# Optimization experiments

Measured on AMD Instinct MI355X. Metric: run time of the kernel, lower is better.

## Reference

```python
import jax, jax.numpy as jnp
import numpy as np
import math

B, C, H, W = 16, 128, 64, 64

def _conv3(x, w, b):
    # 3x3 conv, padding=1 (SAME), NCHW / OIHW
    y = jax.lax.conv_general_dilated(x, w, window_strides=(1, 1), padding='SAME',
                                     dimension_numbers=('NCHW', 'OIHW', 'NCHW'))
    return y + b[None, :, None, None]

def setup_inputs() -> dict:
    key = jax.random.key(0)
    ks = jax.random.split(key, 12)
    s = 0.02
    inp = {
        'F_in': jax.random.normal(ks[0], (B, C, H, W), dtype=jnp.float32),
        'Pspe': jax.random.normal(ks[1], (B, C, C), dtype=jnp.float32),
        'q_w': jax.random.normal(ks[2], (C, C, 3, 3), dtype=jnp.float32) * s,
        'q_b': jnp.zeros((C,), dtype=jnp.float32),
        'k_w': jax.random.normal(ks[3], (C, C, 3, 3), dtype=jnp.float32) * s,
        'k_b': jnp.zeros((C,), dtype=jnp.float32),
        'v_w': jax.random.normal(ks[4], (C, C, 3, 3), dtype=jnp.float32) * s,
        'v_b': jnp.zeros((C,), dtype=jnp.float32),
        'f1_w': jax.random.normal(ks[5], (C, C, 3, 3), dtype=jnp.float32) * s,
        'f1_b': jnp.zeros((C,), dtype=jnp.float32),
        'f2_w': jax.random.normal(ks[6], (C, C, 3, 3), dtype=jnp.float32) * s,
        'f2_b': jnp.zeros((C,), dtype=jnp.float32),
    }
    return inp

def reference(F_in, Pspe, q_w, q_b, k_w, k_b, v_w, v_b, f1_w, f1_b, f2_w, f2_b):
    b, c, h, w = F_in.shape
    hw = h * w
    Qm = _conv3(F_in, q_w, q_b)
    Km = _conv3(F_in, k_w, k_b)
    Vm = _conv3(F_in, v_w, v_b)
    # (B,C,H,W) -> (B,HW,C)
    Q = jnp.transpose(Qm, (0, 2, 3, 1)).reshape(b, hw, c)
    K = jnp.transpose(Km, (0, 2, 3, 1)).reshape(b, hw, c)
    V = jnp.transpose(Vm, (0, 2, 3, 1)).reshape(b, hw, c)
    # channel-wise attention: (B,C,C) = K^T Q, contracting over HW
    attn_logits = jnp.einsum('bnc,bnd->bcd', K, Q) / math.sqrt(hw)
    A = jax.nn.softmax(attn_logits, axis=-1)
    M = jnp.einsum('bce,bed->bcd', Pspe, A)         # prompt fusion
    F3 = jnp.einsum('bnc,bcd->bnd', V, M)           # (B,HW,C)
    F3_map = jnp.transpose(F3.reshape(b, h, w, c), (0, 3, 1, 2))
    # MScanBlock is not defined in the provided source -> identity
    F_ssm = F3_map
    ffn = _conv3(jax.nn.gelu(_conv3(F_ssm, f1_w, f1_b), approximate=False), f2_w, f2_b)
    return F_ssm + ffn
```

## Files before the change

### kernel.cpp

```cpp
#include <hip/hip_runtime.h>
#include <cmath>

typedef unsigned short u16;
typedef __bf16 bf16x8 __attribute__((ext_vector_type(8)));
typedef float f32x4 __attribute__((ext_vector_type(4)));

__device__ __forceinline__ u16 f2bf(float f) {
  unsigned u = __float_as_uint(f);
  u += 0x7fffu + ((u >> 16) & 1u);
  return (u16)(u >> 16);
}
__device__ __forceinline__ float bf2f(u16 h) {
  return __uint_as_float(((unsigned)h) << 16);
}
__device__ __forceinline__ f32x4 mfma_bf16(bf16x8 a, bf16x8 b, f32x4 c) {
  return __builtin_amdgcn_mfma_f32_16x16x32_bf16(a, b, c, 0, 0, 0);
}
__device__ __forceinline__ float gelu_exact(float x) {
  return 0.5f * x * (1.0f + erff(x * 0.70710678118654752440f));
}

#define ROWB 272

__global__ __launch_bounds__(256) void pack_xw(
    const float* __restrict__ Fin, u16* __restrict__ X,
    const float* __restrict__ w0, const float* __restrict__ w1,
    const float* __restrict__ w2, const float* __restrict__ w3,
    const float* __restrict__ w4, u16* __restrict__ Wpk) {
  __shared__ float T[64 * 129];
  const int tid = threadIdx.x;
  if (blockIdx.x < 1024) {
    const int b = blockIdx.x >> 6, y = blockIdx.x & 63;
#pragma unroll
    for (int i = 0; i < 32; ++i) {
      int idx = tid + i * 256;
      int c = idx >> 6, x = idx & 63;
      T[x * 129 + c] = Fin[(size_t)(b * 128 + c) * 4096 + y * 64 + x];
    }
    __syncthreads();
#pragma unroll
    for (int i = 0; i < 4; ++i) {
      int chunk = tid + i * 256;
      int x = chunk >> 4;
      int c0 = (chunk & 15) * 8;
      u16 tmp[8];
#pragma unroll
      for (int e = 0; e < 8; ++e) tmp[e] = f2bf(T[x * 129 + c0 + e]);
      *reinterpret_cast<uint4*>(X + ((size_t)((b * 64 + y) * 64 + x) * 128 + c0)) =
          *reinterpret_cast<const uint4*>(tmp);
    }
  } else {
    int gid = (blockIdx.x - 1024) * 256 + tid;
    int lane = gid & 63;
    int nblk = (gid >> 6) & 7;
    int step = (gid >> 9) % 36;
    int conv = gid / (512 * 36);
    if (conv >= 5) return;
    const float* w = conv == 0 ? w0 : conv == 1 ? w1 : conv == 2 ? w2 : conv == 3 ? w3 : w4;
    int tap = step >> 2, cc = step & 3;
    int dy = tap / 3, dx = tap % 3;
    int co = nblk * 16 + (lane & 15);
    int ci0 = cc * 32 + (lane >> 4) * 8;
    u16 tmp[8];
#pragma unroll
    for (int e = 0; e < 8; ++e)
      tmp[e] = f2bf(w[((size_t)(co * 128 + ci0 + e) * 3 + dy) * 3 + dx]);
    size_t off = ((size_t)conv * 36 * 8 * 64 + (size_t)((step * 8 + nblk) * 64 + lane)) * 8;
    *reinterpret_cast<uint4*>(Wpk + off) = *reinterpret_cast<const uint4*>(tmp);
  }
}

__device__ __forceinline__ void stage_tile(const u16* __restrict__ Xin, char* Xsb,
                                           int tid, int b, int y0) {
#pragma unroll
  for (int i = 0; i < 16; ++i) {
    int j = tid + i * 256;
    int row = j >> 4;
    int c16 = j & 15;
    int ys = row >> 6, x = row & 63;
    int ysrc = y0 - 1 + ys;
    uint4 val = make_uint4(0u, 0u, 0u, 0u);
    if ((unsigned)ysrc < 64u)
      val = *reinterpret_cast<const uint4*>(
          Xin + ((size_t)((b * 64 + ysrc) * 64 + x) * 128 + c16 * 8));
    *reinterpret_cast<uint4*>(Xsb + (ys * 66 + x + 1) * ROWB + c16 * 16) = val;
  }
  if (tid < 128) {
    int ys = tid >> 5, side = (tid >> 4) & 1, c16 = tid & 15;
    int xs = side ? 65 : 0;
    *reinterpret_cast<uint4*>(Xsb + (ys * 66 + xs) * ROWB + c16 * 16) =
        make_uint4(0u, 0u, 0u, 0u);
  }
}

__global__ __launch_bounds__(256, 2) void conv_qkv(
    const u16* __restrict__ Xin, const u16* __restrict__ Wp,
    const float* __restrict__ qb, const float* __restrict__ kb,
    const float* __restrict__ vb, u16* __restrict__ QP,
    u16* __restrict__ KP, u16* __restrict__ Vout) {
  __shared__ alignas(16) char Xsb[4 * 66 * ROWB];
  const int tid = threadIdx.x;
  const int lane = tid & 63;
  const int wv = tid >> 6;
  const int wm = wv >> 1, wn = wv & 1;
  int mt = blockIdx.x;
  mt = (mt & 7) * 128 + (mt >> 3);
  const int b = mt >> 6;
  const int r = mt & 63;
  const int yp = r >> 1;
  const int nh = r & 1;
  const int y0 = yp * 2;

  stage_tile(Xin, Xsb, tid, b, y0);
  __syncthreads();

  f32x4 acc[3][4][2];
#pragma unroll
  for (int c = 0; c < 3; ++c)
#pragma unroll
    for (int i = 0; i < 4; ++i)
#pragma unroll
      for (int j = 0; j < 2; ++j) acc[c][i][j] = f32x4{0.f, 0.f, 0.f, 0.f};

  const int lm = lane & 15, lq = lane >> 4;
  const int abase = lm * ROWB + lq * 16;
  const u16* wb = Wp + (size_t)(((nh * 4 + wn * 2) * 64) + lane) * 8;

  auto loada = [&](bf16x8 (&d)[4], int s) {
    int tap = s >> 2, cc = s & 3;
    int dy = (tap * 11) >> 5;
    int dx = tap - dy * 3;
    int roff = ((wm + dy) * 66 + dx) * ROWB + cc * 64 + abase;
#pragma unroll
    for (int i = 0; i < 4; ++i)
      d[i] = *reinterpret_cast<const bf16x8*>(Xsb + roff + i * (16 * ROWB));
  };
  auto loadb = [&](bf16x8 (&d)[6], int s) {
#pragma unroll
    for (int cv = 0; cv < 3; ++cv)
#pragma unroll
      for (int j = 0; j < 2; ++j)
        d[cv * 2 + j] = *reinterpret_cast<const bf16x8*>(
            wb + (size_t)cv * 147456 + (size_t)s * 4096 + j * 512);
  };
  auto step = [&](bf16x8 (&a)[4], bf16x8 (&bm)[6]) {
#pragma unroll
    for (int cv = 0; cv < 3; ++cv)
#pragma unroll
      for (int i = 0; i < 4; ++i)
#pragma unroll
        for (int j = 0; j < 2; ++j)
          acc[cv][i][j] = mfma_bf16(a[i], bm[cv * 2 + j], acc[cv][i][j]);
  };

  bf16x8 a0[4], a1[4], a2[4], b0[6], b1[6], b2[6];
  loada(a0, 0); loadb(b0, 0);
  loada(a1, 1); loadb(b1, 1);
  loada(a2, 2); loadb(b2, 2);
#pragma unroll 1
  for (int s = 0; s < 36; s += 3) {
    step(a0, b0);
    if (s + 3 < 36) { loada(a0, s + 3); loadb(b0, s + 3); }
    step(a1, b1);
    if (s + 4 < 36) { loada(a1, s + 4); loadb(b1, s + 4); }
    step(a2, b2);
    if (s + 5 < 36) { loada(a2, s + 5); loadb(b2, s + 5); }
  }

  __syncthreads();

  u16* T = reinterpret_cast<u16*>(Xsb);
#pragma unroll
  for (int cv = 0; cv < 2; ++cv) {
    const float* bias = cv == 0 ? qb : kb;
    u16* OutB = cv == 0 ? QP : KP;
#pragma unroll
    for (int i = 0; i < 4; ++i)
#pragma unroll
      for (int j = 0; j < 2; ++j) {
        int nloc = wn * 32 + j * 16 + lm;
        float bs = bias[nh * 64 + nloc];
#pragma unroll
        for (int rr = 0; rr < 4; ++rr) {
          int m = wm * 64 + i * 16 + lq * 4 + rr;
          T[nloc * 136 + m] = f2bf(acc[cv][i][j][rr] + bs);
        }
      }
    __syncthreads();
#pragma unroll
    for (int it = 0; it < 4; ++it) {
      int item = tid + it * 256;
      int l = item & 63, cbl = (item >> 6) & 3, ksl = item >> 8;
      int c = cbl * 16 + (l & 15);
      int mloc = ksl * 32 + (l >> 4) * 8;
      int ks = yp * 4 + ksl, cb = nh * 4 + cbl;
      *reinterpret_cast<uint4*>(
          OutB + (size_t)(((b * 128 + ks) * 8 + cb) * 64 + l) * 8) =
          *reinterpret_cast<const uint4*>(T + c * 136 + mloc);
    }
    __syncthreads();
  }

  u16* Tv = reinterpret_cast<u16*>(Xsb);
#pragma unroll
  for (int i = 0; i < 4; ++i)
#pragma unroll
    for (int j = 0; j < 2; ++j) {
      int nloc = wn * 32 + j * 16 + lm;
      float bs = vb[nh * 64 + nloc];
#pragma unroll
      for (int rr = 0; rr < 4; ++rr) {
        int m = wm * 64 + i * 16 + lq * 4 + rr;
        Tv[m * 72 + nloc] = f2bf(acc[2][i][j][rr] + bs);
      }
    }
  __syncthreads();
  {
    int rr = tid >> 1, q = tid & 1;
    const uint4* src = reinterpret_cast<const uint4*>(Tv + rr * 72 + q * 32);
    uint4* dst = reinterpret_cast<uint4*>(
        Vout + ((size_t)((b * 32 + yp) * 128 + rr) * 128 + nh * 64 + q * 32));
#pragma unroll
    for (int k = 0; k < 4; ++k) dst[k] = src[k];
  }
}

template <int MODE>
__global__ __launch_bounds__(256, 2) void conv_gemm(
    const u16* __restrict__ Xin, const u16* __restrict__ Wp,
    const float* __restrict__ bias, u16* __restrict__ OutB,
    float* __restrict__ OutF, const u16* __restrict__ Vin,
    const u16* __restrict__ Mpk) {
  __shared__ alignas(16) char Xsb[4 * 66 * ROWB];
  const int tid = threadIdx.x;
  const int lane = tid & 63;
  const int wv = tid >> 6;
  const int wm = wv >> 1, wn = wv & 1;
  int mt = blockIdx.x;
  mt = (mt & 7) * 64 + (mt >> 3);
  const int b = mt >> 5;
  const int y0 = (mt & 31) * 2;

  stage_tile(Xin, Xsb, tid, b, y0);
  __syncthreads();

  f32x4 acc[4][4];
#pragma unroll
  for (int i = 0; i < 4; ++i)
#pragma unroll
    for (int j = 0; j < 4; ++j) acc[i][j] = f32x4{0.f, 0.f, 0.f, 0.f};

  const int lm = lane & 15, lq = lane >> 4;
  const int abase = lm * ROWB + lq * 16;
  const u16* wb = Wp + (MODE == 1 ? (size_t)b * 147456 : (size_t)0) +
                  (size_t)((wn * 4 * 64) + lane) * 8;

  auto loada = [&](bf16x8 (&d)[4], int s) {
    int tap = s >> 2, cc = s & 3;
    int dy = (tap * 11) >> 5;
    int dx = tap - dy * 3;
    int roff = ((wm + dy) * 66 + dx) * ROWB + cc * 64 + abase;
#pragma unroll
    for (int i = 0; i < 4; ++i)
      d[i] = *reinterpret_cast<const bf16x8*>(Xsb + roff + i * (16 * ROWB));
  };
  auto loadb = [&](bf16x8 (&d)[4], int s) {
#pragma unroll
    for (int j = 0; j < 4; ++j)
      d[j] = *reinterpret_cast<const bf16x8*>(wb + (size_t)s * 4096 + j * 512);
  };
  auto step = [&](bf16x8 (&a)[4], bf16x8 (&bm)[4]) {
#pragma unroll
    for (int i = 0; i < 4; ++i)
#pragma unroll
      for (int j = 0; j < 4; ++j) acc[i][j] = mfma_bf16(a[i], bm[j], acc[i][j]);
  };

  bf16x8 a0[4], a1[4], a2[4], b0[4], b1[4], b2[4];
  loada(a0, 0); loadb(b0, 0);
  loada(a1, 1); loadb(b1, 1);
  loada(a2, 2); loadb(b2, 2);
#pragma unroll 1
  for (int s = 0; s < 36; s += 3) {
    step(a0, b0);
    if (s + 3 < 36) { loada(a0, s + 3); loadb(b0, s + 3); }
    step(a1, b1);
    if (s + 4 < 36) { loada(a1, s + 4); loadb(b1, s + 4); }
    step(a2, b2);
    if (s + 5 < 36) { loada(a2, s + 5); loadb(b2, s + 5); }
  }

  __syncthreads();

  if (MODE == 1) {
    u16* T = reinterpret_cast<u16*>(Xsb);
#pragma unroll
    for (int i = 0; i < 4; ++i)
#pragma unroll
      for (int j = 0; j < 4; ++j) {
        int n = wn * 64 + j * 16 + lm;
        float bs = bias[n];
#pragma unroll
        for (int r = 0; r < 4; ++r) {
          int m = wm * 64 + i * 16 + lq * 4 + r;
          T[m * 136 + n] = f2bf(gelu_exact(acc[i][j][r] + bs));
        }
      }
    __syncthreads();
    int rr = tid >> 1, hf = tid & 1;
    const uint4* src = reinterpret_cast<const uint4*>(T + rr * 136 + hf * 64);
    uint4* dst = reinterpret_cast<uint4*>(OutB + ((size_t)(mt * 128 + rr) * 128 + hf * 64));
#pragma unroll
    for (int k = 0; k < 8; ++k) dst[k] = src[k];
  } else {
    f32x4 accR[4][4];
#pragma unroll
    for (int i = 0; i < 4; ++i)
#pragma unroll
      for (int j = 0; j < 4; ++j) accR[i][j] = f32x4{0.f, 0.f, 0.f, 0.f};
#pragma unroll
    for (int cc = 0; cc < 4; ++cc) {
      int k0 = cc * 32 + lq * 8;
      bf16x8 af[4], bfr[4];
#pragma unroll
      for (int i = 0; i < 4; ++i)
        af[i] = *reinterpret_cast<const bf16x8*>(
            Vin + (size_t)(mt * 128 + wm * 64 + i * 16 + lm) * 128 + k0);
#pragma unroll
      for (int j = 0; j < 4; ++j)
        bfr[j] = *reinterpret_cast<const bf16x8*>(
            Mpk + (size_t)b * 16384 + (size_t)((cc * 8 + wn * 4 + j) * 64 + lane) * 8);
#pragma unroll
      for (int i = 0; i < 4; ++i)
#pragma unroll
        for (int j = 0; j < 4; ++j) accR[i][j] = mfma_bf16(af[i], bfr[j], accR[i][j]);
    }

    float* T = reinterpret_cast<float*>(Xsb);
#pragma unroll
    for (int i = 0; i < 4; ++i)
#pragma unroll
      for (int j = 0; j < 4; ++j) {
        int n = wn * 64 + j * 16 + lm;
        float bs = bias[n];
#pragma unroll
        for (int r = 0; r < 4; ++r) {
          int m = wm * 64 + i * 16 + lq * 4 + r;
          T[n * 132 + m] = acc[i][j][r] + bs + accR[i][j][r];
        }
      }
    __syncthreads();
    int rr = tid >> 1, hf = tid & 1;
    const uint4* src = reinterpret_cast<const uint4*>(T + rr * 132 + hf * 64);
    uint4* dst = reinterpret_cast<uint4*>(
        OutF + ((size_t)(b * 128 + rr) * 4096 + (mt & 31) * 128 + hf * 64));
#pragma unroll
    for (int k = 0; k < 16; ++k) dst[k] = src[k];
  }
}

__global__ __launch_bounds__(256, 2) void attn_s(const u16* __restrict__ QP,
                                                 const u16* __restrict__ KP,
                                                 float* __restrict__ SP) {
  const int tid = threadIdx.x;
  const int lane = tid & 63;
  const int wv = tid >> 6, wm = wv >> 1, wn = wv & 1;
  const int lm = lane & 15, lq = lane >> 4;
  int mt = blockIdx.x;
  mt = (mt & 7) * 16 + (mt >> 3);
  const int b = mt >> 3, sp = mt & 7;

  f32x4 acc[4][4];
#pragma unroll
  for (int i = 0; i < 4; ++i)
#pragma unroll
    for (int j = 0; j < 4; ++j) acc[i][j] = f32x4{0.f, 0.f, 0.f, 0.f};

#pragma unroll
  for (int ksl = 0; ksl < 16; ++ksl) {
    const int ks = sp * 16 + ksl;
    bf16x8 af[4], bfr[4];
#pragma unroll
    for (int i = 0; i < 4; ++i)
      af[i] = *reinterpret_cast<const bf16x8*>(
          KP + (size_t)(((b * 128 + ks) * 8 + wm * 4 + i) * 64 + lane) * 8);
#pragma unroll
    for (int j = 0; j < 4; ++j)
      bfr[j] = *reinterpret_cast<const bf16x8*>(
          QP + (size_t)(((b * 128 + ks) * 8 + wn * 4 + j) * 64 + lane) * 8);
#pragma unroll
    for (int i = 0; i < 4; ++i)
#pragma unroll
      for (int j = 0; j < 4; ++j) acc[i][j] = mfma_bf16(af[i], bfr[j], acc[i][j]);
  }

  float* out = SP + (size_t)(b * 8 + sp) * 16384;
#pragma unroll
  for (int i = 0; i < 4; ++i)
#pragma unroll
    for (int j = 0; j < 4; ++j)
#pragma unroll
      for (int r = 0; r < 4; ++r)
        out[(wm * 64 + i * 16 + lq * 4 + r) * 128 + wn * 64 + j * 16 + lm] =
            acc[i][j][r];
}

__global__ __launch_bounds__(256, 1) void attn_rm(const float* __restrict__ SP,
                                                  const float* __restrict__ Pspe,
                                                  u16* __restrict__ Mpack,
                                                  u16* __restrict__ Mpack2) {
  __shared__ float Sf[128 * 129];
  __shared__ u16 AT[128 * 136];
  const int b = blockIdx.x;
  const int tid = threadIdx.x;
  const int lane = tid & 63;
  const int wv = tid >> 6, wm = wv >> 1, wn = wv & 1;
  const int lm = lane & 15, lq = lane >> 4;

#pragma unroll
  for (int it = 0; it < 64; ++it) {
    int id = it * 256 + tid;
    int rl = id >> 7, d = id & 127;
    const float* p = SP + (size_t)b * 8 * 16384 + (size_t)rl * 128 + d;
    float s = 0.f;
#pragma unroll
    for (int sp = 0; sp < 8; ++sp) s += p[(size_t)sp * 16384];
    Sf[rl * 129 + d] = s * 0.015625f;
  }
  __syncthreads();

  {
    int c = tid >> 1, hf = tid & 1;
    float* row = Sf + c * 129 + hf * 64;
    float mx = -3.4e38f;
#pragma unroll
    for (int k = 0; k < 64; ++k) mx = fmaxf(mx, row[k]);
    mx = fmaxf(mx, __shfl_xor(mx, 1));
    float s = 0.f;
#pragma unroll
    for (int k = 0; k < 64; ++k) {
      float e = __expf(row[k] - mx);
      row[k] = e;
      s += e;
    }
    s += __shfl_xor(s, 1);
    float inv = 1.0f / s;
#pragma unroll
    for (int k = 0; k < 64; ++k) AT[(hf * 64 + k) * 136 + c] = f2bf(row[k] * inv);
  }
  __syncthreads();

  f32x4 acc2[4][4];
#pragma unroll
  for (int i = 0; i < 4; ++i)
#pragma unroll
    for (int j = 0; j < 4; ++j) acc2[i][j] = f32x4{0.f, 0.f, 0.f, 0.f};
  const float* P = Pspe + (size_t)b * 128 * 128;
#pragma unroll
  for (int cc = 0; cc < 4; ++cc) {
    int e0 = cc * 32 + lq * 8;
    bf16x8 af[4], bfr[4];
#pragma unroll
    for (int i = 0; i < 4; ++i) {
      const float* p = P + (size_t)(wm * 64 + i * 16 + lm) * 128 + e0;
      union { u16 u[8]; bf16x8 v; } cvt;
#pragma unroll
      for (int e = 0; e < 8; ++e) cvt.u[e] = f2bf(p[e]);
      af[i] = cvt.v;
    }
#pragma unroll
    for (int j = 0; j < 4; ++j)
      bfr[j] = *reinterpret_cast<const bf16x8*>(AT + (wn * 64 + j * 16 + lm) * 136 + e0);
#pragma unroll
    for (int i = 0; i < 4; ++i)
#pragma unroll
      for (int j = 0; j < 4; ++j) acc2[i][j] = mfma_bf16(af[i], bfr[j], acc2[i][j]);
  }

  u16* Ml = reinterpret_cast<u16*>(Sf);
#pragma unroll
  for (int i = 0; i < 4; ++i)
#pragma unroll
    for (int j = 0; j < 4; ++j)
#pragma unroll
      for (int r = 0; r < 4; ++r)
        Ml[(wn * 64 + j * 16 + lm) * 136 + (wm * 64 + i * 16 + lq * 4 + r)] =
            f2bf(acc2[i][j][r]);
  __syncthreads();

#pragma unroll
  for (int it = 0; it < 8; ++it) {
    int item = tid + it * 256;
    int l2 = item & 63, nb = (item >> 6) & 7, cc2 = item >> 9;
    int d = nb * 16 + (l2 & 15), c0 = cc2 * 32 + (l2 >> 4) * 8;
    *reinterpret_cast<uint4*>(Mpack + (size_t)b * 16384 + (size_t)item * 8) =
        *reinterpret_cast<const uint4*>(Ml + d * 136 + c0);
  }
#pragma unroll
  for (int it = 0; it < 8; ++it) {
    int item = tid + it * 256;
    int l2 = item & 63, nb = (item >> 6) & 7, cc2 = item >> 9;
    int c = nb * 16 + (l2 & 15), d0 = cc2 * 32 + (l2 >> 4) * 8;
    u16 tmp[8];
#pragma unroll
    for (int e = 0; e < 8; ++e) tmp[e] = Ml[(d0 + e) * 136 + c];
    *reinterpret_cast<uint4*>(Mpack2 + (size_t)b * 16384 + (size_t)item * 8) =
        *reinterpret_cast<const uint4*>(tmp);
  }
}

__global__ __launch_bounds__(256, 2) void wfold1(const u16* __restrict__ W1pk,
                                                 const u16* __restrict__ Mpk2,
                                                 u16* __restrict__ Wf1) {
  __shared__ u16 T[128 * 136];
  const int tid = threadIdx.x;
  const int lane = tid & 63, wv = tid >> 6;
  const int wm = wv >> 1, wn = wv & 1;
  const int lm = lane & 15, lq = lane >> 4;
  const int b = blockIdx.x / 9, tap = blockIdx.x % 9;

  f32x4 acc[4][4];
#pragma unroll
  for (int i = 0; i < 4; ++i)
#pragma unroll
    for (int j = 0; j < 4; ++j) acc[i][j] = f32x4{0.f, 0.f, 0.f, 0.f};

#pragma unroll
  for (int cc = 0; cc < 4; ++cc) {
    bf16x8 af[4], bfr[4];
#pragma unroll
    for (int i = 0; i < 4; ++i)
      af[i] = *reinterpret_cast<const bf16x8*>(
          W1pk + (size_t)(((tap * 4 + cc) * 8 + wm * 4 + i) * 64 + lane) * 8);
#pragma unroll
    for (int j = 0; j < 4; ++j)
      bfr[j] = *reinterpret_cast<const bf16x8*>(
          Mpk2 + (size_t)b * 16384 + (size_t)((cc * 8 + wn * 4 + j) * 64 + lane) * 8);
#pragma unroll
    for (int i = 0; i < 4; ++i)
#pragma unroll
      for (int j = 0; j < 4; ++j) acc[i][j] = mfma_bf16(af[i], bfr[j], acc[i][j]);
  }

#pragma unroll
  for (int i = 0; i < 4; ++i)
#pragma unroll
    for (int j = 0; j < 4; ++j)
#pragma unroll
      for (int r = 0; r < 4; ++r)
        T[(wm * 64 + i * 16 + lq * 4 + r) * 136 + wn * 64 + j * 16 + lm] =
            f2bf(acc[i][j][r]);
  __syncthreads();

#pragma unroll
  for (int it = 0; it < 8; ++it) {
    int item = tid + it * 256;
    int L = item & 63, nb = (item >> 6) & 7, cc2 = item >> 9;
    int co = nb * 16 + (L & 15);
    int c0 = cc2 * 32 + (L >> 4) * 8;
    *reinterpret_cast<uint4*>(
        Wf1 + (size_t)b * 147456 +
        ((size_t)(((tap * 4 + cc2) * 8 + nb) * 64 + L)) * 8) =
        *reinterpret_cast<const uint4*>(T + co * 136 + c0);
  }
}

extern "C" void kernel_launch(void* const* d_in, const int* in_sizes, int n_in,
                              void* d_out, int out_size, void* d_ws, size_t ws_size,
                              hipStream_t stream) {
  const float* F_in = (const float*)d_in[0];
  const float* Pspe = (const float*)d_in[1];
  const float* q_w = (const float*)d_in[2];
  const float* q_b = (const float*)d_in[3];
  const float* k_w = (const float*)d_in[4];
  const float* k_b = (const float*)d_in[5];
  const float* v_w = (const float*)d_in[6];
  const float* v_b = (const float*)d_in[7];
  const float* f1_w = (const float*)d_in[8];
  const float* f1_b = (const float*)d_in[9];
  const float* f2_w = (const float*)d_in[10];
  const float* f2_b = (const float*)d_in[11];
  float* out = (float*)d_out;

  char* ws = (char*)d_ws;
  const size_t SZ = 16777216;
  u16* X = (u16*)(ws);
  u16* QP = (u16*)(ws + SZ);
  u16* KP = (u16*)(ws + 2 * SZ);
  u16* V = (u16*)(ws + 3 * SZ);
  u16* Wpk = (u16*)(ws + 4 * SZ);
  u16* Mpk = (u16*)(ws + 4 * SZ + 1474560);
  u16* Mpk2 = (u16*)(ws + 4 * SZ + 1998848);
  u16* Wf1 = (u16*)(ws + 4 * SZ + 2523136);
  float* SP = (float*)ws;
  u16* Hid = QP;

  pack_xw<<<1384, 256, 0, stream>>>(F_in, X, q_w, k_w, v_w, f1_w, f2_w, Wpk);
  conv_qkv<<<1024, 256, 0, stream>>>(X, Wpk, q_b, k_b, v_b, QP, KP, V);
  attn_s<<<128, 256, 0, stream>>>(QP, KP, SP);
  attn_rm<<<16, 256, 0, stream>>>(SP, Pspe, Mpk, Mpk2);
  wfold1<<<144, 256, 0, stream>>>(Wpk + 3 * 147456, Mpk2, Wf1);
  conv_gemm<1><<<512, 256, 0, stream>>>(V, Wf1, f1_b, Hid, nullptr, nullptr,
                                        nullptr);
  conv_gemm<3><<<512, 256, 0, stream>>>(Hid, Wpk + 4 * 147456, f2_b, nullptr,
                                        out, V, Mpk);
}
```

Before: 170.5 us.

## Halve conv LDS tile by staging input channels in two halves with register prefetch

The conv kernels now stage the 4x66 input halo tile 64 channels at a time instead of all 128, shrinking the LDS row stride from 272 to 144 bytes. This roughly halves shared memory per block, aiming at more resident blocks per CU. The second channel half is loaded into registers while the first half is computed, then written to LDS after a barrier. The fp32 epilogue of the last conv is split into two passes to fit the smaller buffer, and sched_barriers are added to the MFMA loop. The cost is extra barriers, more registers for the prefetch buffer and a serial write gap between the two halves.

Result: slower. 180.0 us (+5.5%).

```diff
diff --git a/kernel.cpp b/kernel.cpp
--- a/kernel.cpp
+++ b/kernel.cpp
@@ -20,7 +20,7 @@
   return 0.5f * x * (1.0f + erff(x * 0.70710678118654752440f));
 }
 
-#define ROWB 272
+#define ROWB 144
 
 __global__ __launch_bounds__(256) void pack_xw(
     const float* __restrict__ Fin, u16* __restrict__ X,
@@ -67,29 +67,6 @@
       tmp[e] = f2bf(w[((size_t)(co * 128 + ci0 + e) * 3 + dy) * 3 + dx]);
     size_t off = ((size_t)conv * 36 * 8 * 64 + (size_t)((step * 8 + nblk) * 64 + lane)) * 8;
     *reinterpret_cast<uint4*>(Wpk + off) = *reinterpret_cast<const uint4*>(tmp);
-  }
-}
-
-__device__ __forceinline__ void stage_tile(const u16* __restrict__ Xin, char* Xsb,
-                                           int tid, int b, int y0) {
-#pragma unroll
-  for (int i = 0; i < 16; ++i) {
-    int j = tid + i * 256;
-    int row = j >> 4;
-    int c16 = j & 15;
-    int ys = row >> 6, x = row & 63;
-    int ysrc = y0 - 1 + ys;
-    uint4 val = make_uint4(0u, 0u, 0u, 0u);
-    if ((unsigned)ysrc < 64u)
-      val = *reinterpret_cast<const uint4*>(
-          Xin + ((size_t)((b * 64 + ysrc) * 64 + x) * 128 + c16 * 8));
-    *reinterpret_cast<uint4*>(Xsb + (ys * 66 + x + 1) * ROWB + c16 * 16) = val;
-  }
-  if (tid < 128) {
-    int ys = tid >> 5, side = (tid >> 4) & 1, c16 = tid & 15;
-    int xs = side ? 65 : 0;
-    *reinterpret_cast<uint4*>(Xsb + (ys * 66 + xs) * ROWB + c16 * 16) =
-        make_uint4(0u, 0u, 0u, 0u);
   }
 }
 
@@ -111,9 +88,6 @@
   const int nh = r & 1;
   const int y0 = yp * 2;
 
-  stage_tile(Xin, Xsb, tid, b, y0);
-  __syncthreads();
-
   f32x4 acc[3][4][2];
 #pragma unroll
   for (int c = 0; c < 3; ++c)
@@ -126,8 +100,38 @@
   const int abase = lm * ROWB + lq * 16;
   const u16* wb = Wp + (size_t)(((nh * 4 + wn * 2) * 64) + lane) * 8;
 
+  uint4 hold[8];
+  auto stage_load = [&](int h) {
+#pragma unroll
+    for (int i = 0; i < 8; ++i) {
+      int j = tid + i * 256;
+      int row = j >> 3, c8 = j & 7;
+      int ys = row >> 6, x = row & 63;
+      int ysrc = y0 - 1 + ys;
+      hold[i] = make_uint4(0u, 0u, 0u, 0u);
+      if ((unsigned)ysrc < 64u)
+        hold[i] = *reinterpret_cast<const uint4*>(
+            Xin + ((size_t)((b * 64 + ysrc) * 64 + x) * 128 + h * 64 + c8 * 8));
+    }
+  };
+  auto stage_write = [&]() {
+#pragma unroll
+    for (int i = 0; i < 8; ++i) {
+      int j = tid + i * 256;
+      int row = j >> 3, c8 = j & 7;
+      int ys = row >> 6, x = row & 63;
+      *reinterpret_cast<uint4*>(Xsb + (ys * 66 + x + 1) * ROWB + c8 * 16) = hold[i];
+    }
+    if (tid < 64) {
+      int ys = tid >> 4, side = (tid >> 3) & 1, c8 = tid & 7;
+      int xs = side ? 65 : 0;
+      *reinterpret_cast<uint4*>(Xsb + (ys * 66 + xs) * ROWB + c8 * 16) =
+          make_uint4(0u, 0u, 0u, 0u);
+    }
+  };
+
   auto loada = [&](bf16x8 (&d)[4], int s) {
-    int tap = s >> 2, cc = s & 3;
+    int tap = s >> 1, cc = s & 1;
     int dy = (tap * 11) >> 5;
     int dx = tap - dy * 3;
     int roff = ((wm + dy) * 66 + dx) * ROWB + cc * 64 + abase;
@@ -135,13 +139,15 @@
     for (int i = 0; i < 4; ++i)
       d[i] = *reinterpret_cast<const bf16x8*>(Xsb + roff + i * (16 * ROWB));
   };
-  auto loadb = [&](bf16x8 (&d)[6], int s) {
+  auto loadb = [&](bf16x8 (&d)[6], int s, int h) {
+    int tap = s >> 1, cc = s & 1;
+    int ws = tap * 4 + h * 2 + cc;
 #pragma unroll
     for (int cv = 0; cv < 3; ++cv)
 #pragma unroll
       for (int j = 0; j < 2; ++j)
         d[cv * 2 + j] = *reinterpret_cast<const bf16x8*>(
-            wb + (size_t)cv * 147456 + (size_t)s * 4096 + j * 512);
+            wb + (size_t)cv * 147456 + (size_t)ws * 4096 + j * 512);
   };
   auto step = [&](bf16x8 (&a)[4], bf16x8 (&bm)[6]) {
 #pragma unroll
@@ -152,20 +158,35 @@
         for (int j = 0; j < 2; ++j)
           acc[cv][i][j] = mfma_bf16(a[i], bm[cv * 2 + j], acc[cv][i][j]);
   };
-
-  bf16x8 a0[4], a1[4], a2[4], b0[6], b1[6], b2[6];
-  loada(a0, 0); loadb(b0, 0);
-  loada(a1, 1); loadb(b1, 1);
-  loada(a2, 2); loadb(b2, 2);
+  auto compute_half = [&](int h) {
+    bf16x8 a0[4], a1[4], a2[4], b0[6], b1[6], b2[6];
+    loada(a0, 0); loadb(b0, 0, h);
+    loada(a1, 1); loadb(b1, 1, h);
+    loada(a2, 2); loadb(b2, 2, h);
 #pragma unroll 1
-  for (int s = 0; s < 36; s += 3) {
-    step(a0, b0);
-    if (s + 3 < 36) { loada(a0, s + 3); loadb(b0, s + 3); }
-    step(a1, b1);
-    if (s + 4 < 36) { loada(a1, s + 4); loadb(b1, s + 4); }
-    step(a2, b2);
-    if (s + 5 < 36) { loada(a2, s + 5); loadb(b2, s + 5); }
-  }
+    for (int s = 0; s < 18; s += 3) {
+      step(a0, b0);
+      { int t = s + 3 < 18 ? s + 3 : 15; loada(a0, t); loadb(b0, t, h); }
+      __builtin_amdgcn_sched_barrier(0);
+      step(a1, b1);
+      { int t = s + 4 < 18 ? s + 4 : 16; loada(a1, t); loadb(b1, t, h); }
+      __builtin_amdgcn_sched_barrier(0);
+      step(a2, b2);
+      { int t = s + 5 < 18 ? s + 5 : 17; loada(a2, t); loadb(b2, t, h); }
+      __builtin_amdgcn_sched_barrier(0);
+    }
+  };
+
+  stage_load(0);
+  stage_write();
+  __syncthreads();
+  stage_load(1);
+  __builtin_amdgcn_sched_barrier(0);
+  compute_half(0);
+  __syncthreads();
+  stage_write();
+  __syncthreads();
+  compute_half(1);
 
   __syncthreads();
 
@@ -239,10 +260,8 @@
   int mt = blockIdx.x;
   mt = (mt & 7) * 64 + (mt >> 3);
   const int b = mt >> 5;
-  const int y0 = (mt & 31) * 2;
-
-  stage_tile(Xin, Xsb, tid, b, y0);
-  __syncthreads();
+  const int yp = mt & 31;
+  const int y0 = yp * 2;
 
   f32x4 acc[4][4];
 #pragma unroll
@@ -255,8 +274,38 @@
   const u16* wb = Wp + (MODE == 1 ? (size_t)b * 147456 : (size_t)0) +
                   (size_t)((wn * 4 * 64) + lane) * 8;
 
+  uint4 hold[8];
+  auto stage_load = [&](int h) {
+#pragma unroll
+    for (int i = 0; i < 8; ++i) {
+      int j = tid + i * 256;
+      int row = j >> 3, c8 = j & 7;
+      int ys = row >> 6, x = row & 63;
+      int ysrc = y0 - 1 + ys;
+      hold[i] = make_uint4(0u, 0u, 0u, 0u);
+      if ((unsigned)ysrc < 64u)
+        hold[i] = *reinterpret_cast<const uint4*>(
+            Xin + ((size_t)((b * 64 + ysrc) * 64 + x) * 128 + h * 64 + c8 * 8));
+    }
+  };
+  auto stage_write = [&]() {
+#pragma unroll
+    for (int i = 0; i < 8; ++i) {
+      int j = tid + i * 256;
+      int row = j >> 3, c8 = j & 7;
+      int ys = row >> 6, x = row & 63;
+      *reinterpret_cast<uint4*>(Xsb + (ys * 66 + x + 1) * ROWB + c8 * 16) = hold[i];
+    }
+    if (tid < 64) {
+      int ys = tid >> 4, side = (tid >> 3) & 1, c8 = tid & 7;
+      int xs = side ? 65 : 0;
+      *reinterpret_cast<uint4*>(Xsb + (ys * 66 + xs) * ROWB + c8 * 16) =
+          make_uint4(0u, 0u, 0u, 0u);
+    }
+  };
+
   auto loada = [&](bf16x8 (&d)[4], int s) {
-    int tap = s >> 2, cc = s & 3;
+    int tap = s >> 1, cc = s & 1;
     int dy = (tap * 11) >> 5;
     int dx = tap - dy * 3;
     int roff = ((wm + dy) * 66 + dx) * ROWB + cc * 64 + abase;
@@ -264,10 +313,12 @@
     for (int i = 0; i < 4; ++i)
       d[i] = *reinterpret_cast<const bf16x8*>(Xsb + roff + i * (16 * ROWB));
   };
-  auto loadb = [&](bf16x8 (&d)[4], int s) {
+  auto loadb = [&](bf16x8 (&d)[4], int s, int h) {
+    int tap = s >> 1, cc = s & 1;
+    int ws = tap * 4 + h * 2 + cc;
 #pragma unroll
     for (int j = 0; j < 4; ++j)
-      d[j] = *reinterpret_cast<const bf16x8*>(wb + (size_t)s * 4096 + j * 512);
+      d[j] = *reinterpret_cast<const bf16x8*>(wb + (size_t)ws * 4096 + j * 512);
   };
   auto step = [&](bf16x8 (&a)[4], bf16x8 (&bm)[4]) {
 #pragma unroll
@@ -275,20 +326,35 @@
 #pragma unroll
       for (int j = 0; j < 4; ++j) acc[i][j] = mfma_bf16(a[i], bm[j], acc[i][j]);
   };
-
-  bf16x8 a0[4], a1[4], a2[4], b0[4], b1[4], b2[4];
-  loada(a0, 0); loadb(b0, 0);
-  loada(a1, 1); loadb(b1, 1);
-  loada(a2, 2); loadb(b2, 2);
+  auto compute_half = [&](int h) {
+    bf16x8 a0[4], a1[4], a2[4], b0[4], b1[4], b2[4];
+    loada(a0, 0); loadb(b0, 0, h);
+    loada(a1, 1); loadb(b1, 1, h);
+    loada(a2, 2); loadb(b2, 2, h);
 #pragma unroll 1
-  for (int s = 0; s < 36; s += 3) {
-    step(a0, b0);
-    if (s + 3 < 36) { loada(a0, s + 3); loadb(b0, s + 3); }
-    step(a1, b1);
-    if (s + 4 < 36) { loada(a1, s + 4); loadb(b1, s + 4); }
-    step(a2, b2);
-    if (s + 5 < 36) { loada(a2, s + 5); loadb(b2, s + 5); }
-  }
+    for (int s = 0; s < 18; s += 3) {
+      step(a0, b0);
+      { int t = s + 3 < 18 ? s + 3 : 15; loada(a0, t); loadb(b0, t, h); }
+      __builtin_amdgcn_sched_barrier(0);
+      step(a1, b1);
+      { int t = s + 4 < 18 ? s + 4 : 16; loada(a1, t); loadb(b1, t, h); }
+      __builtin_amdgcn_sched_barrier(0);
+      step(a2, b2);
+      { int t = s + 5 < 18 ? s + 5 : 17; loada(a2, t); loadb(b2, t, h); }
+      __builtin_amdgcn_sched_barrier(0);
+    }
+  };
+
+  stage_load(0);
+  stage_write();
+  __syncthreads();
+  stage_load(1);
+  __builtin_amdgcn_sched_barrier(0);
+  compute_half(0);
+  __syncthreads();
+  stage_write();
+  __syncthreads();
+  compute_half(1);
 
   __syncthreads();
 
@@ -336,26 +402,33 @@
         for (int j = 0; j < 4; ++j) accR[i][j] = mfma_bf16(af[i], bfr[j], accR[i][j]);
     }
 
-    float* T = reinterpret_cast<float*>(Xsb);
-#pragma unroll
-    for (int i = 0; i < 4; ++i)
-#pragma unroll
-      for (int j = 0; j < 4; ++j) {
-        int n = wn * 64 + j * 16 + lm;
-        float bs = bias[n];
-#pragma unroll
-        for (int r = 0; r < 4; ++r) {
-          int m = wm * 64 + i * 16 + lq * 4 + r;
-          T[n * 132 + m] = acc[i][j][r] + bs + accR[i][j][r];
+    float* Tf = reinterpret_cast<float*>(Xsb);
+#pragma unroll
+    for (int jh = 0; jh < 2; ++jh) {
+      if (jh) __syncthreads();
+#pragma unroll
+      for (int i = 0; i < 4; ++i)
+#pragma unroll
+        for (int j2 = 0; j2 < 2; ++j2) {
+          int j = jh * 2 + j2;
+          int n = wn * 64 + j * 16 + lm;
+          int nl = wn * 32 + j2 * 16 + lm;
+          float bs = bias[n];
+#pragma unroll
+          for (int r = 0; r < 4; ++r) {
+            int m = wm * 64 + i * 16 + lq * 4 + r;
+            Tf[nl * 132 + m] = acc[i][j][r] + bs + accR[i][j][r];
+          }
         }
-      }
-    __syncthreads();
-    int rr = tid >> 1, hf = tid & 1;
-    const uint4* src = reinterpret_cast<const uint4*>(T + rr * 132 + hf * 64);
-    uint4* dst = reinterpret_cast<uint4*>(
-        OutF + ((size_t)(b * 128 + rr) * 4096 + (mt & 31) * 128 + hf * 64));
-#pragma unroll
-    for (int k = 0; k < 16; ++k) dst[k] = src[k];
+      __syncthreads();
+      int nl = tid >> 2, seg = tid & 3;
+      int gn = (nl >> 5) * 64 + jh * 32 + (nl & 31);
+      float* dst = OutF + ((size_t)(b * 128 + gn) * 4096 + yp * 128 + seg * 32);
+      const float* src = Tf + nl * 132 + seg * 32;
+#pragma unroll
+      for (int k = 0; k < 8; ++k)
+        reinterpret_cast<float4*>(dst)[k] = reinterpret_cast<const float4*>(src)[k];
+    }
   }
 }
 
```
